# Kernel tuning notes

Hardware: AMD Instinct MI355X
Metric: run time of the kernel (lower is better)

The kernel has to match this reference:

```python
import jax, jax.numpy as jnp
import numpy as np

B, T = 4, 1024
H, C, DK, DV = 12, 4096, 64, 64
DIM = H * DK  # 768


def setup_inputs() -> dict:
    key = jax.random.key(0)
    k1, k2, k3 = jax.random.split(key, 3)
    x = jax.random.normal(k1, (B, T, DIM), dtype=jnp.float32)
    # key_embed initialized with kaiming_uniform in torch; uniform in [-bound, bound]
    bound = float(np.sqrt(3.0) * np.sqrt(2.0) / np.sqrt(C * DK))
    key_embed = jax.random.uniform(k2, (H, C, DK), minval=-bound, maxval=bound, dtype=jnp.float32)
    values = jax.random.normal(k3, (H, C, DV), dtype=jnp.float32)
    mask = jnp.ones((B, T), dtype=jnp.int32)
    return {"x": x, "mask": mask, "key_embed": key_embed, "values": values, "key_optim": 0}


def reference(x, mask, key_embed, values, key_optim):
    # x: [b, t, h*dk]; key_embed: [h, c, dk]; values: [h, c, dv]
    b, t, _ = x.shape
    h, c, dk = key_embed.shape
    dv = values.shape[-1]
    x = x.astype(jnp.float32)
    # 'b t (h d) -> h (b t) d'
    xh = x.reshape(b, t, h, dk).transpose(2, 0, 1, 3).reshape(h, b * t, dk)
    # squared-L2 nearest codebook entry (argmax of -cdist == argmin of squared dist)
    x2 = jnp.sum(xh * xh, axis=-1, keepdims=True)          # [h, n, 1]
    e2 = jnp.sum(key_embed * key_embed, axis=-1)           # [h, c]
    dots = jnp.einsum('hnd,hcd->hnc', xh, key_embed)       # [h, n, c]
    d2 = x2 - 2.0 * dots + e2[:, None, :]                  # [h, n, c]
    ind = jnp.argmin(d2, axis=-1)                          # [h, n]
    # gather per-head learned values: values[h, ind[h, n], :]
    memories = jnp.take_along_axis(values, ind[..., None], axis=1)  # [h, n, dv]
    # 'h (b t) dv -> b t (h dv)'  (decoder == 'mlp')
    memories = memories.transpose(1, 0, 2).reshape(b, t, h * dv)
    return memories
```

## Files before the change

kernel.cpp:

```cpp
#include <hip/hip_runtime.h>


#define HEADS 12
#define CODES 4096
#define DKI   64
#define DVI   64
#define DIMX  768
#define TAUS  7.68e-3f
#define WLCAP 32768

typedef short bf16x8 __attribute__((ext_vector_type(8)));
typedef _Float16 f16x8 __attribute__((ext_vector_type(8)));
typedef float f32x16 __attribute__((ext_vector_type(16)));

__device__ __forceinline__ unsigned short f2bf(float f) {
    unsigned int u = __float_as_uint(f);
    return (unsigned short)((u + 0x7fff + ((u >> 16) & 1)) >> 16);
}
__device__ __forceinline__ unsigned short f2h(float f) {
    _Float16 h = (_Float16)f;
    unsigned short u;
    __builtin_memcpy(&u, &h, 2);
    return u;
}
__device__ __forceinline__ f16x8 as_f16x8(uint4 v) {
    union { uint4 u; f16x8 h; } c; c.u = v; return c.h;
}

__device__ __forceinline__ float np_sumsq64(const float* __restrict__ a) {
#pragma clang fp contract(off)
    float r[8];
#pragma unroll
    for (int j = 0; j < 8; ++j) r[j] = a[j] * a[j];
#pragma unroll
    for (int i = 8; i < 64; i += 8)
#pragma unroll
        for (int j = 0; j < 8; ++j) r[j] += a[i + j] * a[i + j];
    return ((r[0] + r[1]) + (r[2] + r[3])) + ((r[4] + r[5]) + (r[6] + r[7]));
}

__device__ __forceinline__ float np_dot64(const float* __restrict__ xx,
                                          const float* __restrict__ ee) {
#pragma clang fp contract(off)
    float S0 = 0.f, S1 = 0.f, S2 = 0.f, S3 = 0.f;
#pragma unroll
    for (int t = 0; t < 64; t += 16) {
        float p[16];
#pragma unroll
        for (int j = 0; j < 16; ++j) p[j] = xx[t + j] * ee[t + j];
        S0 = p[0] + (p[4] + (p[8]  + (p[12] + S0)));
        S1 = p[1] + (p[5] + (p[9]  + (p[13] + S1)));
        S2 = p[2] + (p[6] + (p[10] + (p[14] + S2)));
        S3 = p[3] + (p[7] + (p[11] + (p[15] + S3)));
    }
    return (S0 + S1) + (S2 + S3);
}

__global__ __launch_bounds__(256) void prep_ke(const float* __restrict__ ke,
                                               uint4* __restrict__ EhT,
                                               float* __restrict__ e2np,
                                               unsigned short* __restrict__ m2bf,
                                               int* __restrict__ wl_count) {
    __shared__ float sq[32][64];
    __shared__ float rr[32][8];
    const int t = threadIdx.x;
    if (blockIdx.x == 0 && t < 2) wl_count[t] = 0;
    const int p = t >> 5, cw = t & 31;
    const int idx = blockIdx.x * 32 + cw;

    float er[8];
    {
        const float4* p4 = reinterpret_cast<const float4*>(
            ke + (size_t)idx * DKI + p * 8);
        float4 v0 = p4[0], v1 = p4[1];
        er[0] = v0.x; er[1] = v0.y; er[2] = v0.z; er[3] = v0.w;
        er[4] = v1.x; er[5] = v1.y; er[6] = v1.z; er[7] = v1.w;
    }
    {
#pragma clang fp contract(off)
#pragma unroll
        for (int j = 0; j < 8; ++j) sq[cw][p * 8 + j] = er[j] * er[j];
    }
    __syncthreads();
    {
#pragma clang fp contract(off)
        float r = sq[cw][p];
#pragma unroll
        for (int k = 1; k < 8; ++k) r = r + sq[cw][k * 8 + p];
        rr[cw][p] = r;
    }
    __syncthreads();
    const int h = idx >> 12, c = idx & 4095;
    const int half = c >> 11, gg = (c & 2047) >> 5;
    const int pair = h * 2 + half;
    if (p == 0) {
#pragma clang fp contract(off)
        float e2 = ((rr[cw][0] + rr[cw][1]) + (rr[cw][2] + rr[cw][3])) +
                   ((rr[cw][4] + rr[cw][5]) + (rr[cw][6] + rr[cw][7]));
        e2np[idx] = e2;
        m2bf[(size_t)pair * 2048 + (c & 2047)] = f2bf(-32.f * e2);
    }

    unsigned int hb[8];
#pragma unroll
    for (int j = 0; j < 8; ++j)
        hb[j] = f2h(er[j] * 64.f);
    uint4 hv;
    hv.x = hb[0] | (hb[1] << 16); hv.y = hb[2] | (hb[3] << 16);
    hv.z = hb[4] | (hb[5] << 16); hv.w = hb[6] | (hb[7] << 16);
    EhT[((size_t)(pair * 64 + gg) * 8 + p) * 32 + cw] = hv;
}

#define MERGE3(v1o, i1o, v2o, i2o, v3o,                                   \
               a1, j1, a2, j2, a3, b1, k1, b2, k2, b3)                    \
    {                                                                     \
        bool t1 = (b1) > (a1);                                            \
        float _l1 = t1 ? (a1) : (b1);  int _k1 = t1 ? (j1) : (k1);        \
        (v1o) = t1 ? (b1) : (a1);      (i1o) = t1 ? (k1) : (j1);          \
        float _s2 = t1 ? (b2) : (a2);  int _u2 = t1 ? (k2) : (j2);        \
        bool t2 = _s2 > _l1;                                              \
        (v2o) = t2 ? _s2 : _l1;        (i2o) = t2 ? _u2 : _k1;            \
        float _l2 = t2 ? _l1 : _s2;                                       \
        float _s3 = t2 ? (t1 ? (b3) : (a3)) : (t1 ? (a2) : (b2));         \
        bool t3 = _s3 > _l2;                                              \
        (v3o) = t3 ? _s3 : _l2;                                           \
    }

__global__ __launch_bounds__(256, 4) void dkvb_pass1(
        const float* __restrict__ x,
        const char* __restrict__ EhT,
        const unsigned short* __restrict__ m2bf,
        const float* __restrict__ values,
        int* __restrict__ wl_count,
        int* __restrict__ wl,
        int* __restrict__ wlc,
        int* __restrict__ wlf,
        unsigned long long* __restrict__ res,
        float* __restrict__ out) {
    __shared__ float sb1[4][32], sb2[4][32], sb3[4][32];
    __shared__ int   sbi[4][32];
    __shared__ int   fin[32];

    const int tid  = threadIdx.x;
    const int h    = blockIdx.x % 12;
    const int qb   = blockIdx.x / 12;
    const int w    = tid >> 6;
    const int lane = tid & 63;
    const int col  = lane & 31;
    const int kh   = lane >> 5;
    const int q0   = qb * 32;
    const int pair = h * 2 + (w >> 1);

    const float* xrow = x + (size_t)(q0 + col) * DIMX + h * DKI;
    f16x8 ah[4];
#pragma unroll
    for (int t = 0; t < 4; ++t) {
        const float* p = xrow + t * 16 + kh * 8;
        float4 v0 = *reinterpret_cast<const float4*>(p);
        float4 v1 = *reinterpret_cast<const float4*>(p + 4);
        f16x8 hv;
        hv[0] = (_Float16)v0.x; hv[1] = (_Float16)v0.y;
        hv[2] = (_Float16)v0.z; hv[3] = (_Float16)v0.w;
        hv[4] = (_Float16)v1.x; hv[5] = (_Float16)v1.y;
        hv[6] = (_Float16)v1.z; hv[7] = (_Float16)v1.w;
        ah[t] = hv;
    }
    const bf16x8 am2 = (bf16x8){(short)(kh ? 0 : 0x3F80), 0, 0, 0, 0, 0, 0, 0};

    const char* gE = EhT + (size_t)pair * 262144 + (size_t)(w & 1) * 131072
                   + (size_t)kh * 512 + (size_t)col * 16;
    const unsigned short* gm = m2bf + (size_t)pair * 2048
                             + (size_t)(w & 1) * 1024 + col;

    f32x16 zacc;
#pragma unroll
    for (int r = 0; r < 16; ++r) zacc[r] = 0.f;

    float bv[16], bv2[16], bv3[16];
#pragma unroll
    for (int r = 0; r < 16; ++r) { bv[r] = -1e30f; bv2[r] = -1e30f; bv3[r] = -1e30f; }

    auto LOADF = [&](int i, uint4& e0, uint4& e1, uint4& e2, uint4& e3,
                     unsigned short& mA) {
        const char* p = gE + (size_t)i * 4096;
        e0 = *reinterpret_cast<const uint4*>(p);
        e1 = *reinterpret_cast<const uint4*>(p + 1024);
        e2 = *reinterpret_cast<const uint4*>(p + 2048);
        e3 = *reinterpret_cast<const uint4*>(p + 3072);
        mA = gm[i * 32];
    };
    auto COMPUTE = [&](int i, uint4 e0, uint4 e1, uint4 e2, uint4 e3,
                       unsigned short mA) {
        bf16x8 bm = (bf16x8){(short)(kh ? 0 : mA), 0, 0, 0, 0, 0, 0, 0};
        f32x16 acc;
        acc = __builtin_amdgcn_mfma_f32_32x32x16_bf16(am2,   bm,          zacc, 0, 0, 0);
        acc = __builtin_amdgcn_mfma_f32_32x32x16_f16 (ah[0], as_f16x8(e0), acc, 0, 0, 0);
        acc = __builtin_amdgcn_mfma_f32_32x32x16_f16 (ah[1], as_f16x8(e1), acc, 0, 0, 0);
        acc = __builtin_amdgcn_mfma_f32_32x32x16_f16 (ah[2], as_f16x8(e2), acc, 0, 0, 0);
        acc = __builtin_amdgcn_mfma_f32_32x32x16_f16 (ah[3], as_f16x8(e3), acc, 0, 0, 0);
        unsigned enc = (unsigned)i;
#pragma unroll
        for (int r = 0; r < 16; ++r) {
            float sp = __uint_as_float(
                (__float_as_uint(acc[r]) & 0xFFFFFFC0u) | enc);
            bv3[r] = __builtin_amdgcn_fmed3f(bv3[r], sp, bv2[r]);
            bv2[r] = __builtin_amdgcn_fmed3f(bv2[r], sp, bv[r]);
            bv[r]  = fmaxf(bv[r], sp);
        }
    };

    uint4 A0, A1, A2, A3, B0, B1, B2, B3;
    unsigned short Am, Bm;
    LOADF(0, A0, A1, A2, A3, Am);
#pragma unroll 1
    for (int i = 0; i < 32; i += 2) {
        LOADF(i + 1, B0, B1, B2, B3, Bm);
        COMPUTE(i, A0, A1, A2, A3, Am);
        if (i + 2 < 32) LOADF(i + 2, A0, A1, A2, A3, Am);
        COMPUTE(i + 1, B0, B1, B2, B3, Bm);
    }

    int bi1[16], bi2[16];
#pragma unroll
    for (int r = 0; r < 16; ++r) {
        bi1[r] = (int)(__float_as_uint(bv[r])  & 63u) * 32 + col + w * 1024;
        bi2[r] = (int)(__float_as_uint(bv2[r]) & 63u) * 32 + col + w * 1024;
    }
#pragma unroll
    for (int r = 0; r < 16; ++r) {
#pragma unroll
        for (int m = 1; m <= 16; m <<= 1) {
            float p1 = __shfl_xor(bv[r],  m, 64);
            float p2 = __shfl_xor(bv2[r], m, 64);
            float p3 = __shfl_xor(bv3[r], m, 64);
            int   q1 = __shfl_xor(bi1[r], m, 64);
            int   q2 = __shfl_xor(bi2[r], m, 64);
            bool t1 = (p1 > bv[r]) || (p1 == bv[r] && q1 < bi1[r]);
            float w1 = t1 ? p1 : bv[r];   int j1 = t1 ? q1 : bi1[r];
            float l1 = t1 ? bv[r] : p1;   int k1 = t1 ? bi1[r] : q1;
            float s2 = t1 ? p2 : bv2[r];  int u2 = t1 ? q2 : bi2[r];
            bool t2 = s2 > l1;
            float w2 = t2 ? s2 : l1;      int j2 = t2 ? u2 : k1;
            float l2 = t2 ? l1 : s2;
            float s3 = t2 ? (t1 ? p3 : bv3[r]) : (t1 ? bv2[r] : p2);
            bool t3 = s3 > l2;
            float w3 = t3 ? s3 : l2;
            bv[r] = w1; bi1[r] = j1;
            bv2[r] = w2; bi2[r] = j2;
            bv3[r] = w3;
        }
    }
    if (col == 0) {
#pragma unroll
        for (int r = 0; r < 16; ++r) {
            int row = (r & 3) + 8 * (r >> 2) + 4 * kh;
            sb1[w][row] = bv[r];
            sb2[w][row] = bv2[r];
            sb3[w][row] = bv3[r];
            sbi[w][row] = (bi1[r] << 16) | bi2[r];
        }
    }
    __syncthreads();

    if (tid < 32) {
        float v1[4], v2[4], v3[4]; int i1[4], i2[4];
#pragma unroll
        for (int qd = 0; qd < 4; ++qd) {
            v1[qd] = sb1[qd][tid]; v2[qd] = sb2[qd][tid]; v3[qd] = sb3[qd][tid];
            int pk = sbi[qd][tid];
            i1[qd] = (pk >> 16) & 0xffff; i2[qd] = pk & 0xffff;
        }
        float m1a, m2a, m3a, m1b, m2b, m3b, V1, V2, V3;
        int j1a, j2a, j1b, j2b, I1, I2;
        MERGE3(m1a, j1a, m2a, j2a, m3a,
               v1[0], i1[0], v2[0], i2[0], v3[0],
               v1[1], i1[1], v2[1], i2[1], v3[1]);
        MERGE3(m1b, j1b, m2b, j2b, m3b,
               v1[2], i1[2], v2[2], i2[2], v3[2],
               v1[3], i1[3], v2[3], i2[3], v3[3]);
        MERGE3(V1, I1, V2, I2, V3,
               m1a, j1a, m2a, j2a, m3a,
               m1b, j1b, m2b, j2b, m3b);
        fin[tid] = I1;
        if (V1 - V2 < TAUS) {
            if (V1 - V3 < TAUS) {
                int slot = atomicAdd(wl_count + 1, 1);
                if (slot < WLCAP) {
                    wlf[slot] = (h << 16) | (q0 + tid);
                    res[slot] = ~0ULL;
                }
            } else {
                int slot = atomicAdd(wl_count, 1);
                if (slot < WLCAP) {
                    wl[slot]  = (h << 16) | (q0 + tid);
                    wlc[slot] = (I1 << 16) | I2;
                }
            }
        }
    }
    __syncthreads();

#pragma unroll
    for (int k = 0; k < 2; ++k) {
        int f   = tid + k * 256;
        int row = f >> 4;
        int cl  = (f & 15) << 2;
        int idx = fin[row];
        float4 v = *reinterpret_cast<const float4*>(
            values + (size_t)h * CODES * DVI + (size_t)idx * DVI + cl);
        *reinterpret_cast<float4*>(
            out + (size_t)(q0 + row) * DIMX + h * DVI + cl) = v;
    }
}

__global__ __launch_bounds__(256) void cand_check(const float* __restrict__ x,
                                                  const float* __restrict__ ke,
                                                  const float* __restrict__ e2np,
                                                  const float* __restrict__ values,
                                                  const int* __restrict__ wl_count,
                                                  const int* __restrict__ wl,
                                                  const int* __restrict__ wlc,
                                                  float* __restrict__ out) {
    __shared__ float xs[4][DKI];
    const int t = threadIdx.x, w = t >> 6, lane = t & 63;
    int cnt = wl_count[0];
    if (cnt > WLCAP) cnt = WLCAP;

    for (int e = blockIdx.x * 4 + w; e < cnt; e += gridDim.x * 4) {
        int ent = wl[e];
        int h = ent >> 16, nq = ent & 0xffff;
        int cp = wlc[e];
        if (lane < 16) {
            float4 v = *reinterpret_cast<const float4*>(
                x + (size_t)nq * DIMX + h * DKI + lane * 4);
            *reinterpret_cast<float4*>(&xs[w][lane * 4]) = v;
        }
        asm volatile("s_waitcnt lgkmcnt(0)" ::: "memory");
        __builtin_amdgcn_sched_barrier(0);

        int i1 = (cp >> 16) & 0xffff, i2 = cp & 0xffff;
        float d2 = 0.f;
        if (lane < 2) {
            int myc = lane ? i2 : i1;
            float er[DKI];
            const float4* p = reinterpret_cast<const float4*>(
                ke + ((size_t)h * CODES + myc) * DKI);
#pragma unroll
            for (int i = 0; i < DKI / 4; ++i) {
                float4 v = p[i];
                er[i * 4 + 0] = v.x; er[i * 4 + 1] = v.y;
                er[i * 4 + 2] = v.z; er[i * 4 + 3] = v.w;
            }
            float x2 = np_sumsq64(xs[w]);
            float dot = np_dot64(xs[w], er);
            {
#pragma clang fp contract(off)
                d2 = (x2 - 2.0f * dot) + e2np[h * CODES + myc];
            }
        }
        float dA = __shfl(d2, 0, 64);
        float dB = __shfl(d2, 1, 64);
        int win = (dB < dA || (dB == dA && i2 < i1)) ? i2 : i1;
        if (lane < 16) {
            float4 v = *reinterpret_cast<const float4*>(
                values + ((size_t)h * CODES + win) * DVI + lane * 4);
            *reinterpret_cast<float4*>(
                out + (size_t)nq * DIMX + h * DVI + lane * 4) = v;
        }
    }
}

__global__ __launch_bounds__(256) void np_full(const float* __restrict__ x,
                                               const float* __restrict__ ke,
                                               const float* __restrict__ e2np,
                                               const int* __restrict__ wl_count,
                                               const int* __restrict__ wlf,
                                               unsigned long long* __restrict__ res) {
    __shared__ float xs[4][DKI];
    const int t = threadIdx.x, w = t >> 6, lane = t & 63;
    int cnt = wl_count[1];
    if (cnt > WLCAP) cnt = WLCAP;
    const int total = cnt * 8;

    for (int wk = blockIdx.x * 4 + w; wk < total; wk += gridDim.x * 4) {
        const int e = wk >> 3, part = wk & 7;
        const int ent = wlf[e];
        const int h = ent >> 16, nq = ent & 0xffff;
        if (lane < 16) {
            float4 v = *reinterpret_cast<const float4*>(
                x + (size_t)nq * DIMX + h * DKI + lane * 4);
            *reinterpret_cast<float4*>(&xs[w][lane * 4]) = v;
        }
        asm volatile("s_waitcnt lgkmcnt(0)" ::: "memory");
        __builtin_amdgcn_sched_barrier(0);

        float x2 = np_sumsq64(xs[w]);
        unsigned long long best = ~0ULL;
#pragma unroll 1
        for (int it = 0; it < 8; ++it) {
            int c = part * 512 + it * 64 + lane;
            float er[DKI];
            const float4* p = reinterpret_cast<const float4*>(
                ke + ((size_t)h * CODES + c) * DKI);
#pragma unroll
            for (int i = 0; i < DKI / 4; ++i) {
                float4 v = p[i];
                er[i * 4 + 0] = v.x; er[i * 4 + 1] = v.y;
                er[i * 4 + 2] = v.z; er[i * 4 + 3] = v.w;
            }
            float dot = np_dot64(xs[w], er);
            float d2;
            {
#pragma clang fp contract(off)
                d2 = (x2 - 2.0f * dot) + e2np[h * CODES + c];
            }
            unsigned u = __float_as_uint(d2);
            unsigned key = (u & 0x80000000u) ? ~u : (u | 0x80000000u);
            unsigned long long pk = ((unsigned long long)key << 32) | (unsigned)c;
            best = pk < best ? pk : best;
        }
#pragma unroll
        for (int m = 1; m <= 32; m <<= 1) {
            unsigned long long o =
                (unsigned long long)__shfl_xor((long long)best, m, 64);
            best = o < best ? o : best;
        }
        if (lane == 0) atomicMin(res + e, best);
    }
}

__global__ __launch_bounds__(256) void np_fin(const float* __restrict__ values,
                                              const int* __restrict__ wl_count,
                                              const int* __restrict__ wlf,
                                              const unsigned long long* __restrict__ res,
                                              float* __restrict__ out) {
    int cnt = wl_count[1];
    if (cnt > WLCAP) cnt = WLCAP;
    const int total = cnt * 16;
    for (int f = blockIdx.x * 256 + threadIdx.x; f < total; f += gridDim.x * 256) {
        int e  = f >> 4;
        int cl = (f & 15) << 2;
        int ent = wlf[e];
        int h = ent >> 16, nq = ent & 0xffff;
        int c = (int)(res[e] & 0xFFFFFFFFULL);
        float4 v = *reinterpret_cast<const float4*>(
            values + ((size_t)h * CODES + c) * DVI + cl);
        *reinterpret_cast<float4*>(
            out + (size_t)nq * DIMX + h * DVI + cl) = v;
    }
}

extern "C" void kernel_launch(void* const* d_in, const int* in_sizes, int n_in,
                              void* d_out, int out_size, void* d_ws, size_t ws_size,
                              hipStream_t stream) {
    const float* x      = (const float*)d_in[0];
    const float* ke     = (const float*)d_in[2];
    const float* values = (const float*)d_in[3];
    float* out = (float*)d_out;

    char* ws = (char*)d_ws;
    float* e2np          = (float*)ws;          ws += (size_t)HEADS * CODES * 4;
    unsigned short* m2bf = (unsigned short*)ws; ws += (size_t)HEADS * 2 * 2048 * 2;
    int*   wl_count      = (int*)ws;            ws += 64;
    int*   wl            = (int*)ws;            ws += (size_t)WLCAP * 4;
    int*   wlc           = (int*)ws;            ws += (size_t)WLCAP * 4;
    int*   wlf           = (int*)ws;            ws += (size_t)WLCAP * 4;
    unsigned long long* res = (unsigned long long*)ws; ws += (size_t)WLCAP * 8;
    char*  EhT           = ws;                  ws += (size_t)HEADS * CODES * 128;

    prep_ke<<<dim3(HEADS * CODES / 32), dim3(256), 0, stream>>>(
        ke, (uint4*)EhT, e2np, m2bf, wl_count);
    dkvb_pass1<<<dim3(1536), dim3(256), 0, stream>>>(
        x, EhT, m2bf, values, wl_count, wl, wlc, wlf, res, out);
    cand_check<<<dim3(1024), dim3(256), 0, stream>>>(
        x, ke, e2np, values, wl_count, wl, wlc, out);
    np_full<<<dim3(1024), dim3(256), 0, stream>>>(
        x, ke, e2np, wl_count, wlf, res);
    np_fin<<<dim3(256), dim3(256), 0, stream>>>(
        values, wl_count, wlf, res, out);
}
```

Before: 197.9 us.

## Merge fallback kernels into one post-check kernel and triple-buffer codebook loads

The candidate check, full nearest-code search and final gather kernels are folded into one post_check kernel. The last of eight partial searches per entry, found through a per-entry atomic counter, writes the winning value row, so two launches are removed. The main pass now keeps three codebook tiles in flight instead of two and lowers its occupancy target from 4 to 3 to make room for the extra registers. The cost is more register pressure and atomic and fence traffic per fallback entry.

```diff
diff --git a/kernel.cpp b/kernel.cpp
--- a/kernel.cpp
+++ b/kernel.cpp
@@ -126,7 +126,7 @@
         (v3o) = t3 ? _s3 : _l2;                                           \
     }
 
-__global__ __launch_bounds__(256, 4) void dkvb_pass1(
+__global__ __launch_bounds__(256, 3) void dkvb_pass1(
         const float* __restrict__ x,
         const char* __restrict__ EhT,
         const unsigned short* __restrict__ m2bf,
@@ -136,6 +136,7 @@
         int* __restrict__ wlc,
         int* __restrict__ wlf,
         unsigned long long* __restrict__ res,
+        int* __restrict__ pcnt,
         float* __restrict__ out) {
     __shared__ float sb1[4][32], sb2[4][32], sb3[4][32];
     __shared__ int   sbi[4][32];
@@ -209,16 +210,21 @@
         }
     };
 
-    uint4 A0, A1, A2, A3, B0, B1, B2, B3;
-    unsigned short Am, Bm;
+    uint4 A0, A1, A2, A3, B0, B1, B2, B3, C0, C1, C2, C3;
+    unsigned short Am, Bm, Cm;
     LOADF(0, A0, A1, A2, A3, Am);
+    LOADF(1, B0, B1, B2, B3, Bm);
 #pragma unroll 1
-    for (int i = 0; i < 32; i += 2) {
-        LOADF(i + 1, B0, B1, B2, B3, Bm);
+    for (int i = 0; i < 30; i += 3) {
+        LOADF(i + 2, C0, C1, C2, C3, Cm);
         COMPUTE(i, A0, A1, A2, A3, Am);
-        if (i + 2 < 32) LOADF(i + 2, A0, A1, A2, A3, Am);
+        LOADF(i + 3, A0, A1, A2, A3, Am);
         COMPUTE(i + 1, B0, B1, B2, B3, Bm);
-    }
+        LOADF(i + 4, B0, B1, B2, B3, Bm);
+        COMPUTE(i + 2, C0, C1, C2, C3, Cm);
+    }
+    COMPUTE(30, A0, A1, A2, A3, Am);
+    COMPUTE(31, B0, B1, B2, B3, Bm);
 
     int bi1[16], bi2[16];
 #pragma unroll
@@ -286,8 +292,9 @@
             if (V1 - V3 < TAUS) {
                 int slot = atomicAdd(wl_count + 1, 1);
                 if (slot < WLCAP) {
-                    wlf[slot] = (h << 16) | (q0 + tid);
-                    res[slot] = ~0ULL;
+                    wlf[slot]  = (h << 16) | (q0 + tid);
+                    res[slot]  = ~0ULL;
+                    pcnt[slot] = 0;
                 }
             } else {
                 int slot = atomicAdd(wl_count, 1);
@@ -313,140 +320,132 @@
     }
 }
 
-__global__ __launch_bounds__(256) void cand_check(const float* __restrict__ x,
+__global__ __launch_bounds__(256) void post_check(const float* __restrict__ x,
                                                   const float* __restrict__ ke,
                                                   const float* __restrict__ e2np,
                                                   const float* __restrict__ values,
                                                   const int* __restrict__ wl_count,
                                                   const int* __restrict__ wl,
                                                   const int* __restrict__ wlc,
+                                                  const int* __restrict__ wlf,
+                                                  unsigned long long* __restrict__ res,
+                                                  int* __restrict__ pcnt,
                                                   float* __restrict__ out) {
     __shared__ float xs[4][DKI];
     const int t = threadIdx.x, w = t >> 6, lane = t & 63;
-    int cnt = wl_count[0];
-    if (cnt > WLCAP) cnt = WLCAP;
-
-    for (int e = blockIdx.x * 4 + w; e < cnt; e += gridDim.x * 4) {
-        int ent = wl[e];
-        int h = ent >> 16, nq = ent & 0xffff;
-        int cp = wlc[e];
-        if (lane < 16) {
-            float4 v = *reinterpret_cast<const float4*>(
-                x + (size_t)nq * DIMX + h * DKI + lane * 4);
-            *reinterpret_cast<float4*>(&xs[w][lane * 4]) = v;
-        }
-        asm volatile("s_waitcnt lgkmcnt(0)" ::: "memory");
-        __builtin_amdgcn_sched_barrier(0);
-
-        int i1 = (cp >> 16) & 0xffff, i2 = cp & 0xffff;
-        float d2 = 0.f;
-        if (lane < 2) {
-            int myc = lane ? i2 : i1;
-            float er[DKI];
-            const float4* p = reinterpret_cast<const float4*>(
-                ke + ((size_t)h * CODES + myc) * DKI);
-#pragma unroll
-            for (int i = 0; i < DKI / 4; ++i) {
-                float4 v = p[i];
-                er[i * 4 + 0] = v.x; er[i * 4 + 1] = v.y;
-                er[i * 4 + 2] = v.z; er[i * 4 + 3] = v.w;
-            }
+    int cnt0 = wl_count[0]; if (cnt0 > WLCAP) cnt0 = WLCAP;
+    int cnt1 = wl_count[1]; if (cnt1 > WLCAP) cnt1 = WLCAP;
+    const int total = cnt0 + cnt1 * 8;
+
+    for (int item = blockIdx.x * 4 + w; item < total; item += gridDim.x * 4) {
+        if (item < cnt0) {
+            int ent = wl[item];
+            int h = ent >> 16, nq = ent & 0xffff;
+            int cp = wlc[item];
+            if (lane < 16) {
+                float4 v = *reinterpret_cast<const float4*>(
+                    x + (size_t)nq * DIMX + h * DKI + lane * 4);
+                *reinterpret_cast<float4*>(&xs[w][lane * 4]) = v;
+            }
+            asm volatile("s_waitcnt lgkmcnt(0)" ::: "memory");
+            __builtin_amdgcn_sched_barrier(0);
+
+            int i1 = (cp >> 16) & 0xffff, i2 = cp & 0xffff;
+            float d2 = 0.f;
+            if (lane < 2) {
+                int myc = lane ? i2 : i1;
+                float er[DKI];
+                const float4* p = reinterpret_cast<const float4*>(
+                    ke + ((size_t)h * CODES + myc) * DKI);
+#pragma unroll
+                for (int i = 0; i < DKI / 4; ++i) {
+                    float4 v = p[i];
+                    er[i * 4 + 0] = v.x; er[i * 4 + 1] = v.y;
+                    er[i * 4 + 2] = v.z; er[i * 4 + 3] = v.w;
+                }
+                float x2 = np_sumsq64(xs[w]);
+                float dot = np_dot64(xs[w], er);
+                {
+#pragma clang fp contract(off)
+                    d2 = (x2 - 2.0f * dot) + e2np[h * CODES + myc];
+                }
+            }
+            float dA = __shfl(d2, 0, 64);
+            float dB = __shfl(d2, 1, 64);
+            int win = (dB < dA || (dB == dA && i2 < i1)) ? i2 : i1;
+            if (lane < 16) {
+                float4 v = *reinterpret_cast<const float4*>(
+                    values + ((size_t)h * CODES + win) * DVI + lane * 4);
+                *reinterpret_cast<float4*>(
+                    out + (size_t)nq * DIMX + h * DVI + lane * 4) = v;
+            }
+        } else {
+            const int j = item - cnt0;
+            const int e = j >> 3, part = j & 7;
+            const int ent = wlf[e];
+            const int h = ent >> 16, nq = ent & 0xffff;
+            if (lane < 16) {
+                float4 v = *reinterpret_cast<const float4*>(
+                    x + (size_t)nq * DIMX + h * DKI + lane * 4);
+                *reinterpret_cast<float4*>(&xs[w][lane * 4]) = v;
+            }
+            asm volatile("s_waitcnt lgkmcnt(0)" ::: "memory");
+            __builtin_amdgcn_sched_barrier(0);
+
             float x2 = np_sumsq64(xs[w]);
-            float dot = np_dot64(xs[w], er);
-            {
-#pragma clang fp contract(off)
-                d2 = (x2 - 2.0f * dot) + e2np[h * CODES + myc];
-            }
-        }
-        float dA = __shfl(d2, 0, 64);
-        float dB = __shfl(d2, 1, 64);
-        int win = (dB < dA || (dB == dA && i2 < i1)) ? i2 : i1;
-        if (lane < 16) {
-            float4 v = *reinterpret_cast<const float4*>(
-                values + ((size_t)h * CODES + win) * DVI + lane * 4);
-            *reinterpret_cast<float4*>(
-                out + (size_t)nq * DIMX + h * DVI + lane * 4) = v;
-        }
-    }
-}
-
-__global__ __launch_bounds__(256) void np_full(const float* __restrict__ x,
-                                               const float* __restrict__ ke,
-                                               const float* __restrict__ e2np,
-                                               const int* __restrict__ wl_count,
-                                               const int* __restrict__ wlf,
-                                               unsigned long long* __restrict__ res) {
-    __shared__ float xs[4][DKI];
-    const int t = threadIdx.x, w = t >> 6, lane = t & 63;
-    int cnt = wl_count[1];
-    if (cnt > WLCAP) cnt = WLCAP;
-    const int total = cnt * 8;
-
-    for (int wk = blockIdx.x * 4 + w; wk < total; wk += gridDim.x * 4) {
-        const int e = wk >> 3, part = wk & 7;
-        const int ent = wlf[e];
-        const int h = ent >> 16, nq = ent & 0xffff;
-        if (lane < 16) {
-            float4 v = *reinterpret_cast<const float4*>(
-                x + (size_t)nq * DIMX + h * DKI + lane * 4);
-            *reinterpret_cast<float4*>(&xs[w][lane * 4]) = v;
-        }
-        asm volatile("s_waitcnt lgkmcnt(0)" ::: "memory");
-        __builtin_amdgcn_sched_barrier(0);
-
-        float x2 = np_sumsq64(xs[w]);
-        unsigned long long best = ~0ULL;
+            unsigned long long best = ~0ULL;
 #pragma unroll 1
-        for (int it = 0; it < 8; ++it) {
-            int c = part * 512 + it * 64 + lane;
-            float er[DKI];
-            const float4* p = reinterpret_cast<const float4*>(
-                ke + ((size_t)h * CODES + c) * DKI);
-#pragma unroll
-            for (int i = 0; i < DKI / 4; ++i) {
-                float4 v = p[i];
-                er[i * 4 + 0] = v.x; er[i * 4 + 1] = v.y;
-                er[i * 4 + 2] = v.z; er[i * 4 + 3] = v.w;
-            }
-            float dot = np_dot64(xs[w], er);
-            float d2;
-            {
-#pragma clang fp contract(off)
-                d2 = (x2 - 2.0f * dot) + e2np[h * CODES + c];
-            }
-            unsigned u = __float_as_uint(d2);
-            unsigned key = (u & 0x80000000u) ? ~u : (u | 0x80000000u);
-            unsigned long long pk = ((unsigned long long)key << 32) | (unsigned)c;
-            best = pk < best ? pk : best;
-        }
-#pragma unroll
-        for (int m = 1; m <= 32; m <<= 1) {
-            unsigned long long o =
-                (unsigned long long)__shfl_xor((long long)best, m, 64);
-            best = o < best ? o : best;
-        }
-        if (lane == 0) atomicMin(res + e, best);
-    }
-}
-
-__global__ __launch_bounds__(256) void np_fin(const float* __restrict__ values,
-                                              const int* __restrict__ wl_count,
-                                              const int* __restrict__ wlf,
-                                              const unsigned long long* __restrict__ res,
-                                              float* __restrict__ out) {
-    int cnt = wl_count[1];
-    if (cnt > WLCAP) cnt = WLCAP;
-    const int total = cnt * 16;
-    for (int f = blockIdx.x * 256 + threadIdx.x; f < total; f += gridDim.x * 256) {
-        int e  = f >> 4;
-        int cl = (f & 15) << 2;
-        int ent = wlf[e];
-        int h = ent >> 16, nq = ent & 0xffff;
-        int c = (int)(res[e] & 0xFFFFFFFFULL);
-        float4 v = *reinterpret_cast<const float4*>(
-            values + ((size_t)h * CODES + c) * DVI + cl);
-        *reinterpret_cast<float4*>(
-            out + (size_t)nq * DIMX + h * DVI + cl) = v;
+            for (int it = 0; it < 8; ++it) {
+                int c = part * 512 + it * 64 + lane;
+                float er[DKI];
+                const float4* p = reinterpret_cast<const float4*>(
+                    ke + ((size_t)h * CODES + c) * DKI);
+#pragma unroll
+                for (int i = 0; i < DKI / 4; ++i) {
+                    float4 v = p[i];
+                    er[i * 4 + 0] = v.x; er[i * 4 + 1] = v.y;
+                    er[i * 4 + 2] = v.z; er[i * 4 + 3] = v.w;
+                }
+                float dot = np_dot64(xs[w], er);
+                float d2;
+                {
+#pragma clang fp contract(off)
+                    d2 = (x2 - 2.0f * dot) + e2np[h * CODES + c];
+                }
+                unsigned u = __float_as_uint(d2);
+                unsigned key = (u & 0x80000000u) ? ~u : (u | 0x80000000u);
+                unsigned long long pk =
+                    ((unsigned long long)key << 32) | (unsigned)c;
+                best = pk < best ? pk : best;
+            }
+#pragma unroll
+            for (int m = 1; m <= 32; m <<= 1) {
+                unsigned long long o =
+                    (unsigned long long)__shfl_xor((long long)best, m, 64);
+                best = o < best ? o : best;
+            }
+            int lastflag = 0;
+            if (lane == 0) {
+                atomicMin(res + e, best);
+                __threadfence();
+                lastflag = (atomicAdd(pcnt + e, 1) == 7);
+            }
+            lastflag = __shfl(lastflag, 0, 64);
+            if (lastflag) {
+                unsigned long long fin = 0;
+                if (lane == 0) {
+                    __threadfence();
+                    fin = atomicMin(res + e, ~0ULL);
+                }
+                int win = (int)(__shfl((long long)fin, 0, 64) & 0xFFFFFFFFLL);
+                if (lane < 16) {
+                    float4 v = *reinterpret_cast<const float4*>(
+                        values + ((size_t)h * CODES + win) * DVI + lane * 4);
+                    *reinterpret_cast<float4*>(
+                        out + (size_t)nq * DIMX + h * DVI + lane * 4) = v;
+                }
+            }
+        }
     }
 }
 
@@ -466,16 +465,13 @@
     int*   wlc           = (int*)ws;            ws += (size_t)WLCAP * 4;
     int*   wlf           = (int*)ws;            ws += (size_t)WLCAP * 4;
     unsigned long long* res = (unsigned long long*)ws; ws += (size_t)WLCAP * 8;
+    int*   pcnt          = (int*)ws;            ws += (size_t)WLCAP * 4;
     char*  EhT           = ws;                  ws += (size_t)HEADS * CODES * 128;
 
     prep_ke<<<dim3(HEADS * CODES / 32), dim3(256), 0, stream>>>(
         ke, (uint4*)EhT, e2np, m2bf, wl_count);
     dkvb_pass1<<<dim3(1536), dim3(256), 0, stream>>>(
-        x, EhT, m2bf, values, wl_count, wl, wlc, wlf, res, out);
-    cand_check<<<dim3(1024), dim3(256), 0, stream>>>(
-        x, ke, e2np, values, wl_count, wl, wlc, out);
-    np_full<<<dim3(1024), dim3(256), 0, stream>>>(
-        x, ke, e2np, wl_count, wlf, res);
-    np_fin<<<dim3(256), dim3(256), 0, stream>>>(
-        values, wl_count, wlf, res, out);
-}
+        x, EhT, m2bf, values, wl_count, wl, wlc, wlf, res, pcnt, out);
+    post_check<<<dim3(1024), dim3(256), 0, stream>>>(
+        x, ke, e2np, values, wl_count, wl, wlc, wlf, res, pcnt, out);
+}
```

Result: faster. 192.6 us (-2.7%).
